# Kernel optimization log

Hardware: AMD Instinct MI355X
Metric: run time of the kernel (lower is better)

The kernel has to match this reference:

```python
import jax, jax.numpy as jnp
import numpy as np

B, T, D = 2, 2048, 2048   # batch, seq, model dim
H = 1408                  # expert hidden dim
E = 16                    # routed experts
S = 2                     # shared experts
TOP_K = 2
SCALE = 0.02


def setup_inputs() -> dict:
    key = jax.random.key(0)
    ks = jax.random.split(key, 6)
    return {
        "x": jax.random.normal(ks[0], (B, T, D), jnp.float32),
        "gate_w": jax.random.normal(ks[1], (D, E), jnp.float32) * SCALE,
        "shared_w1": jax.random.normal(ks[2], (S, D, H), jnp.float32) * SCALE,
        "shared_w2": jax.random.normal(ks[3], (S, H, D), jnp.float32) * SCALE,
        "expert_w1": jax.random.normal(ks[4], (E, D, H), jnp.float32) * SCALE,
        "expert_w2": jax.random.normal(ks[5], (E, H, D), jnp.float32) * SCALE,
    }


def reference(x, gate_w, shared_w1, shared_w2, expert_w1, expert_w2):
    xf = x.reshape(-1, x.shape[-1])            # [T_tot, D]
    n_tok = xf.shape[0]

    # shared experts: sum of SiLU FFNs
    sh = jax.nn.silu(jnp.einsum('td,sdh->sth', xf, shared_w1))
    shared_out = jnp.einsum('sth,shd->td', sh, shared_w2)

    # router
    logits = xf @ gate_w                       # [T_tot, E]
    probs = jax.nn.softmax(logits, axis=-1)
    topk_w, topk_idx = jax.lax.top_k(probs, TOP_K)
    topk_w = topk_w / topk_w.sum(axis=-1, keepdims=True)

    # aux load-balancing loss
    aux_loss = (probs.mean(axis=0) * logits.mean(axis=0)).sum() * E

    # scatter normalized top-k weights into dense [T_tot, E] combine matrix
    combine = jnp.zeros((n_tok, E), xf.dtype).at[
        jnp.arange(n_tok)[:, None], topk_idx
    ].add(topk_w)

    # routed experts computed densely over all tokens, combined by routing weights
    h = jax.nn.silu(jnp.einsum('td,edh->eth', xf, expert_w1))   # [E, T_tot, H]
    eo = jnp.einsum('eth,ehd->etd', h, expert_w2)               # [E, T_tot, D]
    routed_out = jnp.einsum('te,etd->td', combine, eo)

    total = (shared_out + routed_out).reshape(x.shape)
    return total, aux_loss
```

## Files before the change

### kernel.cpp

```cpp
#include <hip/hip_runtime.h>
#include <hip/hip_bf16.h>


#define T_TOT   4096
#define DMODEL  2048
#define HDIM    1408
#define NEXP    16
#define MAXSLOT 10240
#define MAXTILE 80

typedef short     bf16x8_t  __attribute__((ext_vector_type(8)));
typedef float     f32x4_t   __attribute__((ext_vector_type(4)));
typedef ushort    u16x8_t   __attribute__((ext_vector_type(8)));

__device__ __forceinline__ ushort f2bf(float f) {
    unsigned u = __float_as_uint(f);
    u += 0x7fffu + ((u >> 16) & 1u);
    return (ushort)(u >> 16);
}
__device__ __forceinline__ float bf2f(ushort b) { return __uint_as_float((unsigned)b << 16); }
__device__ __forceinline__ float silu(float v) { return v / (1.0f + __expf(-v)); }

__device__ __forceinline__ void async16(const ushort* g, ushort* l) {
    __builtin_amdgcn_global_load_lds((const __attribute__((address_space(1))) void*)g,
                                     (__attribute__((address_space(3))) void*)l, 16, 0, 0);
}


__global__ void init_kernel(int* cnt, double* ps, double* ls) {
    if (threadIdx.x < NEXP) { cnt[threadIdx.x] = 0; ps[threadIdx.x] = 0.0; ls[threadIdx.x] = 0.0; }
}

__global__ __launch_bounds__(256) void cvt_bf16(const float* __restrict__ src, ushort* __restrict__ dst) {
    size_t i = ((size_t)blockIdx.x * 256 + threadIdx.x) * 4;
    float4 v = *(const float4*)(src + i);
    ushort4 o; o.x = f2bf(v.x); o.y = f2bf(v.y); o.z = f2bf(v.z); o.w = f2bf(v.w);
    *(ushort4*)(dst + i) = o;
}

__global__ __launch_bounds__(256) void transpose_cvt(const float* __restrict__ src, ushort* __restrict__ dst,
                                                     int R, int C, long sbatch, long dbatch, int ldd) {
    __shared__ ushort t[64][72];
    const float* s = src + (long)blockIdx.z * sbatch;
    ushort* d = dst + (long)blockIdx.z * dbatch;
    int c0 = blockIdx.x * 64, r0 = blockIdx.y * 64;
    int tx = threadIdx.x & 15, ty = threadIdx.x >> 4;
#pragma unroll
    for (int i = 0; i < 4; i++) {
        int r = ty + i * 16;
        float4 v = *(const float4*)(s + (size_t)(r0 + r) * C + c0 + tx * 4);
        ushort4 o; o.x = f2bf(v.x); o.y = f2bf(v.y); o.z = f2bf(v.z); o.w = f2bf(v.w);
        *(ushort4*)&t[r][tx * 4] = o;
    }
    __syncthreads();
    int cx = threadIdx.x & 7, cy = threadIdx.x >> 3;
#pragma unroll
    for (int i = 0; i < 2; i++) {
        int cc = cy + i * 32;
        u16x8_t o;
#pragma unroll
        for (int j = 0; j < 8; j++) o[j] = t[cx * 8 + j][cc];
        *(u16x8_t*)(d + (size_t)(c0 + cc) * ldd + r0 + cx * 8) = o;
    }
}


__global__ __launch_bounds__(256) void router_kernel(const float* __restrict__ x, const float* __restrict__ gw,
                                                     int* __restrict__ topk_idx, float* __restrict__ topk_w,
                                                     double* __restrict__ probs_sum, double* __restrict__ logits_sum,
                                                     int* __restrict__ cnt) {
    int wv = threadIdx.x >> 6, l = threadIdx.x & 63;
    int t = blockIdx.x * 4 + wv;
    double acc[NEXP];
#pragma unroll
    for (int e = 0; e < NEXP; e++) acc[e] = 0.0;
    const float* xr = x + (size_t)t * DMODEL;
    for (int i = 0; i < DMODEL / 64; i++) {
        int d = i * 64 + l;
        double xv = (double)xr[d];
        const float4* g = (const float4*)(gw + (size_t)d * NEXP);
        float4 g0 = g[0], g1 = g[1], g2 = g[2], g3 = g[3];
        acc[0]  += xv * (double)g0.x; acc[1]  += xv * (double)g0.y;
        acc[2]  += xv * (double)g0.z; acc[3]  += xv * (double)g0.w;
        acc[4]  += xv * (double)g1.x; acc[5]  += xv * (double)g1.y;
        acc[6]  += xv * (double)g1.z; acc[7]  += xv * (double)g1.w;
        acc[8]  += xv * (double)g2.x; acc[9]  += xv * (double)g2.y;
        acc[10] += xv * (double)g2.z; acc[11] += xv * (double)g2.w;
        acc[12] += xv * (double)g3.x; acc[13] += xv * (double)g3.y;
        acc[14] += xv * (double)g3.z; acc[15] += xv * (double)g3.w;
    }
#pragma unroll
    for (int off = 32; off; off >>= 1)
#pragma unroll
        for (int e = 0; e < NEXP; e++) acc[e] += __shfl_down(acc[e], off);

    __shared__ double bp[4][NEXP], bl[4][NEXP];
    if (l == 0) {
        double m = acc[0];
#pragma unroll
        for (int e = 1; e < NEXP; e++) m = acc[e] > m ? acc[e] : m;
        double p[NEXP], s = 0.0;
#pragma unroll
        for (int e = 0; e < NEXP; e++) { p[e] = exp(acc[e] - m); s += p[e]; }
#pragma unroll
        for (int e = 0; e < NEXP; e++) p[e] /= s;
        int e1 = 0;
#pragma unroll
        for (int e = 1; e < NEXP; e++) if (p[e] > p[e1]) e1 = e;
        int e2 = (e1 == 0) ? 1 : 0;
#pragma unroll
        for (int e = 0; e < NEXP; e++) if (e != e1 && p[e] > p[e2]) e2 = e;
        double s2 = p[e1] + p[e2];
        topk_idx[t * 2] = e1; topk_idx[t * 2 + 1] = e2;
        topk_w[t * 2] = (float)(p[e1] / s2); topk_w[t * 2 + 1] = (float)(p[e2] / s2);
        atomicAdd(&cnt[e1], 1); atomicAdd(&cnt[e2], 1);
#pragma unroll
        for (int e = 0; e < NEXP; e++) { bp[wv][e] = p[e]; bl[wv][e] = acc[e]; }
    }
    __syncthreads();
    if (threadIdx.x < NEXP) {
        int e = threadIdx.x;
        atomicAdd(&probs_sum[e], bp[0][e] + bp[1][e] + bp[2][e] + bp[3][e]);
        atomicAdd(&logits_sum[e], bl[0][e] + bl[1][e] + bl[2][e] + bl[3][e]);
    }
}

__global__ void setup_kernel(const int* __restrict__ cnt, int* __restrict__ cursor,
                             int* __restrict__ tile_expert, int* __restrict__ tile_row, int* __restrict__ meta,
                             int* __restrict__ slot_token, float* __restrict__ slot_w,
                             const double* __restrict__ probs_sum, const double* __restrict__ logits_sum,
                             float* __restrict__ out_aux) {
    if (threadIdx.x == 0) {
        int off = 0, nt = 0;
        for (int e = 0; e < NEXP; e++) {
            cursor[e] = off;
            int tiles = (cnt[e] + 127) >> 7;
            for (int j = 0; j < tiles; j++) { tile_expert[nt] = e; tile_row[nt] = off + j * 128; nt++; }
            off += tiles * 128;
        }
        meta[0] = nt; meta[1] = off;
        double aux = 0.0;
        for (int e = 0; e < NEXP; e++)
            aux += (probs_sum[e] / (double)T_TOT) * (logits_sum[e] / (double)T_TOT);
        out_aux[0] = (float)(aux * (double)NEXP);
    }
    __syncthreads();
    for (int i = threadIdx.x; i < MAXSLOT; i += 256) { slot_token[i] = 0; slot_w[i] = 0.0f; }
}

__global__ void scatter_kernel(const int* __restrict__ topk_idx, const float* __restrict__ topk_w,
                               int* __restrict__ cursor, int* __restrict__ slot_token, float* __restrict__ slot_w,
                               int* __restrict__ slot_of) {
    int t = blockIdx.x * 256 + threadIdx.x;
#pragma unroll
    for (int k = 0; k < 2; k++) {
        int e = topk_idx[t * 2 + k];
        int pos = atomicAdd(&cursor[e], 1);
        slot_token[pos] = t;
        slot_w[pos] = topk_w[t * 2 + k];
        slot_of[t * 2 + k] = pos;
    }
}


template<bool INDIRECT_A>
__device__ __forceinline__ void gemm_tile_core(const ushort* __restrict__ A, const ushort* __restrict__ B,
                                               int lda, int ldb, int K, int m0, int n0,
                                               const int* __restrict__ rowmap,
                                               f32x4_t acc[4][4], ushort* lds) {
    const int tid = threadIdx.x;
    const int w = tid >> 6, l = tid & 63;
    const int c0 = w * 2, c1 = c0 + 1;
    const int subrow = l >> 2;
    const int kc = (l & 3) * 8;
    int ar0 = c0 * 16 + subrow, ar1 = c1 * 16 + subrow;
    long ga0, ga1;
    if (INDIRECT_A) { ga0 = (long)rowmap[m0 + ar0]; ga1 = (long)rowmap[m0 + ar1]; }
    else            { ga0 = (long)(m0 + ar0);       ga1 = (long)(m0 + ar1); }
    const ushort* pa0 = A + ga0 * lda + kc;
    const ushort* pa1 = A + ga1 * lda + kc;
    const ushort* pb0 = B + (long)(n0 + ar0) * ldb + kc;
    const ushort* pb1 = B + (long)(n0 + ar1) * ldb + kc;
    const int wm = w & 1, wn = w >> 1;
    const int lrow = l & 15, quad = l >> 4;

    {
        ushort* d0 = lds + c0 * 512;
        ushort* d1 = lds + c1 * 512;
        async16(pa0, d0); async16(pa1, d1);
        async16(pb0, d0 + 4096); async16(pb1, d1 + 4096);
    }
    int cur = 0;
    for (int kt = 0; kt < K; kt += 32) {
        __syncthreads();
        if (kt + 32 < K) {
            pa0 += 32; pa1 += 32; pb0 += 32; pb1 += 32;
            ushort* e0 = lds + (cur ^ 1) * 8192 + c0 * 512;
            ushort* e1 = lds + (cur ^ 1) * 8192 + c1 * 512;
            async16(pa0, e0); async16(pa1, e1);
            async16(pb0, e0 + 4096); async16(pb1, e1 + 4096);
        }
        const ushort* As = lds + cur * 8192;
        const ushort* Bs = As + 4096;
        bf16x8_t a[4], b[4];
#pragma unroll
        for (int mi = 0; mi < 4; mi++)
            a[mi] = *(const bf16x8_t*)(As + (wm * 64 + mi * 16 + lrow) * 32 + quad * 8);
#pragma unroll
        for (int ni = 0; ni < 4; ni++)
            b[ni] = *(const bf16x8_t*)(Bs + (wn * 64 + ni * 16 + lrow) * 32 + quad * 8);
#pragma unroll
        for (int mi = 0; mi < 4; mi++)
#pragma unroll
            for (int ni = 0; ni < 4; ni++)
                acc[mi][ni] = __builtin_amdgcn_mfma_f32_16x16x32_bf16(a[mi], b[ni], acc[mi][ni], 0, 0, 0);
        cur ^= 1;
    }
}

template<int MODE>
__global__ __launch_bounds__(256, 3) void gemm_dense(const ushort* __restrict__ A, const ushort* __restrict__ B,
                                                     void* __restrict__ C, int lda, int ldb, int ldc, int K,
                                                     long bStride, int cZOff) {
    __shared__ ushort lds[16384];
    int m0 = blockIdx.x * 128, n0 = blockIdx.y * 128;
    const ushort* Bz = B + (long)blockIdx.z * bStride;
    f32x4_t acc[4][4];
#pragma unroll
    for (int mi = 0; mi < 4; mi++)
#pragma unroll
        for (int ni = 0; ni < 4; ni++) acc[mi][ni] = (f32x4_t){0.f, 0.f, 0.f, 0.f};
    gemm_tile_core<false>(A, Bz, lda, ldb, K, m0, n0, nullptr, acc, lds);

    const int w = threadIdx.x >> 6, l = threadIdx.x & 63;
    const int wm = w & 1, wn = w >> 1, quad = l >> 4, lcol = l & 15;
    int colBase = (int)blockIdx.z * cZOff + n0 + wn * 64;
#pragma unroll
    for (int mi = 0; mi < 4; mi++) {
        int rowb = m0 + wm * 64 + mi * 16 + quad * 4;
#pragma unroll
        for (int ni = 0; ni < 4; ni++) {
            int col = colBase + ni * 16 + lcol;
#pragma unroll
            for (int r = 0; r < 4; r++) {
                float v = acc[mi][ni][r];
                if (MODE == 0) ((ushort*)C)[(long)(rowb + r) * ldc + col] = f2bf(silu(v));
                else           ((float*)C)[(long)(rowb + r) * ldc + col] = v;
            }
        }
    }
}

template<int MODE>
__global__ __launch_bounds__(256, 3) void gemm_grouped(const ushort* __restrict__ A, const ushort* __restrict__ B,
                                                       void* __restrict__ C, int lda, int ldb, int ldc, int K,
                                                       long bExpertStride,
                                                       const int* __restrict__ tile_expert,
                                                       const int* __restrict__ tile_row,
                                                       const int* __restrict__ meta,
                                                       const int* __restrict__ slot_token,
                                                       const float* __restrict__ slot_w) {
    if ((int)blockIdx.x >= meta[0]) return;
    __shared__ ushort lds[16384];
    int e = tile_expert[blockIdx.x];
    int m0 = tile_row[blockIdx.x];
    int n0 = blockIdx.y * 128;
    const ushort* Be = B + (long)e * bExpertStride;
    f32x4_t acc[4][4];
#pragma unroll
    for (int mi = 0; mi < 4; mi++)
#pragma unroll
        for (int ni = 0; ni < 4; ni++) acc[mi][ni] = (f32x4_t){0.f, 0.f, 0.f, 0.f};
    gemm_tile_core<MODE == 1>(A, Be, lda, ldb, K, m0, n0, slot_token, acc, lds);

    const int w = threadIdx.x >> 6, l = threadIdx.x & 63;
    const int wm = w & 1, wn = w >> 1, quad = l >> 4, lcol = l & 15;
#pragma unroll
    for (int mi = 0; mi < 4; mi++) {
        int rowb = m0 + wm * 64 + mi * 16 + quad * 4;
#pragma unroll
        for (int ni = 0; ni < 4; ni++) {
            int col = n0 + wn * 64 + ni * 16 + lcol;
#pragma unroll
            for (int r = 0; r < 4; r++) {
                float v = acc[mi][ni][r];
                int row = rowb + r;
                if (MODE == 1) {
                    ((ushort*)C)[(long)row * ldc + col] = f2bf(silu(v));
                } else {
                    float wt = slot_w[row];
                    ((ushort*)C)[(long)row * ldc + col] = f2bf(v * wt);
                }
            }
        }
    }
}

__global__ __launch_bounds__(256) void combine_kernel(float* __restrict__ out, const ushort* __restrict__ ro,
                                                      const int* __restrict__ slot_of) {
    int t = blockIdx.x;
    int s1 = slot_of[t * 2], s2 = slot_of[t * 2 + 1];
    const u16x8_t* r1 = (const u16x8_t*)(ro + (size_t)s1 * DMODEL);
    const u16x8_t* r2 = (const u16x8_t*)(ro + (size_t)s2 * DMODEL);
    int i = threadIdx.x;
    u16x8_t a = r1[i], b = r2[i];
    float4* o = (float4*)(out + (size_t)t * DMODEL) + i * 2;
    float4 o0 = o[0], o1 = o[1];
    o0.x += bf2f(a[0]) + bf2f(b[0]); o0.y += bf2f(a[1]) + bf2f(b[1]);
    o0.z += bf2f(a[2]) + bf2f(b[2]); o0.w += bf2f(a[3]) + bf2f(b[3]);
    o1.x += bf2f(a[4]) + bf2f(b[4]); o1.y += bf2f(a[5]) + bf2f(b[5]);
    o1.z += bf2f(a[6]) + bf2f(b[6]); o1.w += bf2f(a[7]) + bf2f(b[7]);
    o[0] = o0; o[1] = o1;
}


extern "C" void kernel_launch(void* const* d_in, const int* in_sizes, int n_in,
                              void* d_out, int out_size, void* d_ws, size_t ws_size,
                              hipStream_t stream) {
    const float* x   = (const float*)d_in[0];
    const float* gw  = (const float*)d_in[1];
    const float* sw1 = (const float*)d_in[2];
    const float* sw2 = (const float*)d_in[3];
    const float* ew1 = (const float*)d_in[4];
    const float* ew2 = (const float*)d_in[5];
    float* out = (float*)d_out;

    char* p = (char*)d_ws;
    auto alloc = [&](size_t bytes) { char* r = p; p += (bytes + 511) & ~(size_t)511; return r; };
    ushort* xb    = (ushort*)alloc((size_t)T_TOT * DMODEL * 2);
    ushort* w1t   = (ushort*)alloc((size_t)2 * HDIM * DMODEL * 2);
    ushort* w2t   = (ushort*)alloc((size_t)DMODEL * 2 * HDIM * 2);
    ushort* ew1t  = (ushort*)alloc((size_t)NEXP * HDIM * DMODEL * 2);
    ushort* ew2t  = (ushort*)alloc((size_t)NEXP * DMODEL * HDIM * 2);
    ushort* h     = (ushort*)alloc((size_t)T_TOT * 2 * HDIM * 2);
    ushort* hg    = (ushort*)alloc((size_t)MAXSLOT * HDIM * 2);
    ushort* ro    = (ushort*)alloc((size_t)MAXSLOT * DMODEL * 2);
    int*    slot_token = (int*)alloc(MAXSLOT * 4);
    float*  slot_w     = (float*)alloc(MAXSLOT * 4);
    int*    slot_of    = (int*)alloc(T_TOT * 2 * 4);
    int*    topk_idx   = (int*)alloc(T_TOT * 2 * 4);
    float*  topk_w     = (float*)alloc(T_TOT * 2 * 4);
    int*    cnt        = (int*)alloc(64);
    int*    cursor     = (int*)alloc(64);
    int*    tile_expert= (int*)alloc(512);
    int*    tile_row   = (int*)alloc(512);
    int*    meta       = (int*)alloc(64);
    double* probs_sum  = (double*)alloc(128);
    double* logits_sum = (double*)alloc(128);

    init_kernel<<<1, 64, 0, stream>>>(cnt, probs_sum, logits_sum);
    cvt_bf16<<<(T_TOT * DMODEL) / 1024, 256, 0, stream>>>(x, xb);
    transpose_cvt<<<dim3(HDIM / 64, DMODEL / 64, 2), 256, 0, stream>>>(
        sw1, w1t, DMODEL, HDIM, (long)DMODEL * HDIM, (long)HDIM * DMODEL, DMODEL);
    transpose_cvt<<<dim3(DMODEL / 64, HDIM / 64, 2), 256, 0, stream>>>(
        sw2, w2t, HDIM, DMODEL, (long)HDIM * DMODEL, (long)HDIM, 2 * HDIM);
    transpose_cvt<<<dim3(HDIM / 64, DMODEL / 64, NEXP), 256, 0, stream>>>(
        ew1, ew1t, DMODEL, HDIM, (long)DMODEL * HDIM, (long)HDIM * DMODEL, DMODEL);
    transpose_cvt<<<dim3(DMODEL / 64, HDIM / 64, NEXP), 256, 0, stream>>>(
        ew2, ew2t, HDIM, DMODEL, (long)HDIM * DMODEL, (long)DMODEL * HDIM, HDIM);

    router_kernel<<<T_TOT / 4, 256, 0, stream>>>(x, gw, topk_idx, topk_w, probs_sum, logits_sum, cnt);
    setup_kernel<<<1, 256, 0, stream>>>(cnt, cursor, tile_expert, tile_row, meta,
                                        slot_token, slot_w, probs_sum, logits_sum, out + (size_t)T_TOT * DMODEL);
    scatter_kernel<<<T_TOT / 256, 256, 0, stream>>>(topk_idx, topk_w, cursor, slot_token, slot_w, slot_of);

    gemm_dense<0><<<dim3(T_TOT / 128, HDIM / 128, 2), 256, 0, stream>>>(
        xb, w1t, h, DMODEL, DMODEL, 2 * HDIM, DMODEL, (long)HDIM * DMODEL, HDIM);
    gemm_grouped<1><<<dim3(MAXTILE, HDIM / 128), 256, 0, stream>>>(
        xb, ew1t, hg, DMODEL, DMODEL, HDIM, DMODEL, (long)HDIM * DMODEL,
        tile_expert, tile_row, meta, slot_token, slot_w);
    gemm_dense<2><<<dim3(T_TOT / 128, DMODEL / 128, 1), 256, 0, stream>>>(
        h, w2t, out, 2 * HDIM, 2 * HDIM, DMODEL, 2 * HDIM, 0L, 0);
    gemm_grouped<3><<<dim3(MAXTILE, DMODEL / 128), 256, 0, stream>>>(
        hg, ew2t, ro, HDIM, HDIM, DMODEL, HDIM, (long)DMODEL * HDIM,
        tile_expert, tile_row, meta, slot_token, slot_w);
    combine_kernel<<<T_TOT, 256, 0, stream>>>(out, ro, slot_of);
}
```

Measured before the change: 957.9 us.

## Rewrite router with fp32 accumulation, two tokens per wave, vectorized loads

The router GEMV now accumulates partial dot products in fp32 instead of fp64. Each wave handles two tokens so every gate-weight load is reused, and both x and the gate weights are read as float4. The per-token reduction moves into shared memory and a 16-lane shuffle softmax and top-2, with the final sums still done in fp64. The aim is to cut the fp64 arithmetic and the redundant gate-weight traffic in the router. The cost is slightly different rounding in the logits, which could flip top-k choices when two experts are nearly tied.

```diff
diff --git a/kernel.cpp b/kernel.cpp
--- a/kernel.cpp
+++ b/kernel.cpp
@@ -69,59 +69,100 @@
                                                      int* __restrict__ topk_idx, float* __restrict__ topk_w,
                                                      double* __restrict__ probs_sum, double* __restrict__ logits_sum,
                                                      int* __restrict__ cnt) {
-    int wv = threadIdx.x >> 6, l = threadIdx.x & 63;
-    int t = blockIdx.x * 4 + wv;
-    double acc[NEXP];
-#pragma unroll
-    for (int e = 0; e < NEXP; e++) acc[e] = 0.0;
-    const float* xr = x + (size_t)t * DMODEL;
-    for (int i = 0; i < DMODEL / 64; i++) {
-        int d = i * 64 + l;
-        double xv = (double)xr[d];
-        const float4* g = (const float4*)(gw + (size_t)d * NEXP);
-        float4 g0 = g[0], g1 = g[1], g2 = g[2], g3 = g[3];
-        acc[0]  += xv * (double)g0.x; acc[1]  += xv * (double)g0.y;
-        acc[2]  += xv * (double)g0.z; acc[3]  += xv * (double)g0.w;
-        acc[4]  += xv * (double)g1.x; acc[5]  += xv * (double)g1.y;
-        acc[6]  += xv * (double)g1.z; acc[7]  += xv * (double)g1.w;
-        acc[8]  += xv * (double)g2.x; acc[9]  += xv * (double)g2.y;
-        acc[10] += xv * (double)g2.z; acc[11] += xv * (double)g2.w;
-        acc[12] += xv * (double)g3.x; acc[13] += xv * (double)g3.y;
-        acc[14] += xv * (double)g3.z; acc[15] += xv * (double)g3.w;
-    }
-#pragma unroll
-    for (int off = 32; off; off >>= 1)
-#pragma unroll
-        for (int e = 0; e < NEXP; e++) acc[e] += __shfl_down(acc[e], off);
-
-    __shared__ double bp[4][NEXP], bl[4][NEXP];
-    if (l == 0) {
-        double m = acc[0];
-#pragma unroll
-        for (int e = 1; e < NEXP; e++) m = acc[e] > m ? acc[e] : m;
-        double p[NEXP], s = 0.0;
-#pragma unroll
-        for (int e = 0; e < NEXP; e++) { p[e] = exp(acc[e] - m); s += p[e]; }
-#pragma unroll
-        for (int e = 0; e < NEXP; e++) p[e] /= s;
-        int e1 = 0;
-#pragma unroll
-        for (int e = 1; e < NEXP; e++) if (p[e] > p[e1]) e1 = e;
-        int e2 = (e1 == 0) ? 1 : 0;
-#pragma unroll
-        for (int e = 0; e < NEXP; e++) if (e != e1 && p[e] > p[e2]) e2 = e;
-        double s2 = p[e1] + p[e2];
-        topk_idx[t * 2] = e1; topk_idx[t * 2 + 1] = e2;
-        topk_w[t * 2] = (float)(p[e1] / s2); topk_w[t * 2 + 1] = (float)(p[e2] / s2);
-        atomicAdd(&cnt[e1], 1); atomicAdd(&cnt[e2], 1);
-#pragma unroll
-        for (int e = 0; e < NEXP; e++) { bp[wv][e] = p[e]; bl[wv][e] = acc[e]; }
+    const int wv = threadIdx.x >> 6, l = threadIdx.x & 63;
+    const int tBase = blockIdx.x * 8 + wv * 2;
+
+    float acc0[NEXP], acc1[NEXP];
+#pragma unroll
+    for (int e = 0; e < NEXP; e++) { acc0[e] = 0.f; acc1[e] = 0.f; }
+
+    const float* x0 = x + (size_t)tBase * DMODEL;
+    const float* x1 = x0 + DMODEL;
+
+#pragma unroll
+    for (int i = 0; i < 8; i++) {
+        const int d0 = i * 256 + l * 4;
+        float4 xa = *(const float4*)(x0 + d0);
+        float4 xb = *(const float4*)(x1 + d0);
+        const float4* g = (const float4*)(gw + (size_t)d0 * NEXP);
+        float gf[64];
+#pragma unroll
+        for (int j = 0; j < 16; j++) {
+            float4 t = g[j];
+            gf[4 * j] = t.x; gf[4 * j + 1] = t.y; gf[4 * j + 2] = t.z; gf[4 * j + 3] = t.w;
+        }
+        const float xs0[4] = {xa.x, xa.y, xa.z, xa.w};
+        const float xs1[4] = {xb.x, xb.y, xb.z, xb.w};
+#pragma unroll
+        for (int r = 0; r < 4; r++)
+#pragma unroll
+            for (int e = 0; e < NEXP; e++) {
+                acc0[e] += xs0[r] * gf[r * 16 + e];
+                acc1[e] += xs1[r] * gf[r * 16 + e];
+            }
+    }
+
+#pragma unroll
+    for (int e = 0; e < NEXP; e++) {
+        acc0[e] += __shfl_xor(acc0[e], 32); acc0[e] += __shfl_xor(acc0[e], 16);
+        acc1[e] += __shfl_xor(acc1[e], 32); acc1[e] += __shfl_xor(acc1[e], 16);
+    }
+
+    __shared__ float  sred[4][2][16][17];
+    __shared__ double sp[4][2][NEXP], sl[4][2][NEXP];
+
+    if (l < 16) {
+#pragma unroll
+        for (int e = 0; e < NEXP; e++) { sred[wv][0][l][e] = acc0[e]; sred[wv][1][l][e] = acc1[e]; }
     }
     __syncthreads();
+
+    if (l < 32) {
+        const int tok = l >> 4, e = l & 15;
+        double lg = 0.0;
+#pragma unroll
+        for (int g = 0; g < 16; g++) lg += (double)sred[wv][tok][g][e];
+
+        double m = lg;
+#pragma unroll
+        for (int off = 8; off; off >>= 1) { double o = __shfl_xor(m, off); m = o > m ? o : m; }
+        double pe = exp(lg - m);
+        double ss = pe;
+#pragma unroll
+        for (int off = 8; off; off >>= 1) ss += __shfl_xor(ss, off);
+        double p = pe / ss;
+
+        double v = p; int ie = e;
+#pragma unroll
+        for (int off = 8; off; off >>= 1) {
+            double ov = __shfl_xor(v, off); int oi = __shfl_xor(ie, off);
+            if (ov > v || (ov == v && oi < ie)) { v = ov; ie = oi; }
+        }
+        double v2 = (e == ie) ? -1.0 : p; int ie2 = e;
+#pragma unroll
+        for (int off = 8; off; off >>= 1) {
+            double ov = __shfl_xor(v2, off); int oi = __shfl_xor(ie2, off);
+            if (ov > v2 || (ov == v2 && oi < ie2)) { v2 = ov; ie2 = oi; }
+        }
+
+        sp[wv][tok][e] = p; sl[wv][tok][e] = lg;
+
+        if (e == 0) {
+            int t = tBase + tok;
+            double s2 = v + v2;
+            topk_idx[t * 2] = ie;  topk_idx[t * 2 + 1] = ie2;
+            topk_w[t * 2] = (float)(v / s2); topk_w[t * 2 + 1] = (float)(v2 / s2);
+            atomicAdd(&cnt[ie], 1); atomicAdd(&cnt[ie2], 1);
+        }
+    }
+    __syncthreads();
+
     if (threadIdx.x < NEXP) {
         int e = threadIdx.x;
-        atomicAdd(&probs_sum[e], bp[0][e] + bp[1][e] + bp[2][e] + bp[3][e]);
-        atomicAdd(&logits_sum[e], bl[0][e] + bl[1][e] + bl[2][e] + bl[3][e]);
+        double ps = 0.0, ls = 0.0;
+#pragma unroll
+        for (int w = 0; w < 4; w++) { ps += sp[w][0][e] + sp[w][1][e]; ls += sl[w][0][e] + sl[w][1][e]; }
+        atomicAdd(&probs_sum[e], ps); atomicAdd(&logits_sum[e], ls);
     }
 }
 
@@ -359,7 +400,7 @@
     transpose_cvt<<<dim3(DMODEL / 64, HDIM / 64, NEXP), 256, 0, stream>>>(
         ew2, ew2t, HDIM, DMODEL, (long)HDIM * DMODEL, (long)DMODEL * HDIM, HDIM);
 
-    router_kernel<<<T_TOT / 4, 256, 0, stream>>>(x, gw, topk_idx, topk_w, probs_sum, logits_sum, cnt);
+    router_kernel<<<T_TOT / 8, 256, 0, stream>>>(x, gw, topk_idx, topk_w, probs_sum, logits_sum, cnt);
     setup_kernel<<<1, 256, 0, stream>>>(cnt, cursor, tile_expert, tile_row, meta,
                                         slot_token, slot_w, probs_sum, logits_sum, out + (size_t)T_TOT * DMODEL);
     scatter_kernel<<<T_TOT / 256, 256, 0, stream>>>(topk_idx, topk_w, cursor, slot_token, slot_w, slot_of);
```

Measured after the change: 914.0 us. 1.05x faster.
